# Kernel optimization log

Measured on AMD Instinct MI355X. Metric: run time of the kernel, lower is better.

Reference implementation:

```python
import jax, jax.numpy as jnp
import numpy as np

B, T, N, D, C = 32, 256, 256, 1024, 80
SIM_THRESH = 0.7
MAX_AGE = 10
W_SIM, W_IOU = 0.7, 0.3


def setup_inputs() -> dict:
    key = jax.random.key(0)
    ks = jax.random.split(key, 8)
    track_memory = jax.random.normal(ks[0], (B, T, D), jnp.float32)
    track_boxes = jax.random.uniform(ks[1], (B, T, 4), jnp.float32, 0.05, 0.95)
    track_active = jax.random.bernoulli(ks[2], 0.9, (B, T))
    track_age = jax.random.randint(ks[3], (B, T), 0, 5, jnp.int32)
    track_hits = jax.random.randint(ks[4], (B, T), 1, 10, jnp.int32)
    det_boxes = jax.random.uniform(ks[5], (B, N, 4), jnp.float32, 0.05, 0.95)
    # correlate detections with tracks so cosine similarity exceeds the
    # matching threshold for many pairs and the greedy loop does real work
    det_memory = track_memory + 0.3 * jax.random.normal(ks[6], (B, N, D), jnp.float32)
    class_logits = jax.random.normal(ks[7], (B, N, C), jnp.float32)
    return {
        'track_memory': track_memory, 'track_boxes': track_boxes,
        'track_active': track_active, 'track_age': track_age,
        'track_hits': track_hits, 'det_boxes': det_boxes,
        'det_memory': det_memory, 'class_logits': class_logits,
    }


def _normalize(x):
    # matches F.normalize(dim=-1): x / max(||x||, eps)
    n = jnp.linalg.norm(x, axis=-1, keepdims=True)
    return x / jnp.maximum(n, 1e-12)


def _iou_matrix(tb, db):
    # tb [T,4], db [N,4], boxes in (cx, cy, w, h) format -> IoU [T,N]
    t_x1, t_y1 = tb[:, 0] - tb[:, 2] / 2, tb[:, 1] - tb[:, 3] / 2
    t_x2, t_y2 = tb[:, 0] + tb[:, 2] / 2, tb[:, 1] + tb[:, 3] / 2
    d_x1, d_y1 = db[:, 0] - db[:, 2] / 2, db[:, 1] - db[:, 3] / 2
    d_x2, d_y2 = db[:, 0] + db[:, 2] / 2, db[:, 1] + db[:, 3] / 2
    iw = jnp.clip(jnp.minimum(t_x2[:, None], d_x2[None, :]) - jnp.maximum(t_x1[:, None], d_x1[None, :]), 0.0)
    ih = jnp.clip(jnp.minimum(t_y2[:, None], d_y2[None, :]) - jnp.maximum(t_y1[:, None], d_y1[None, :]), 0.0)
    inter = iw * ih
    union = (tb[:, 2] * tb[:, 3])[:, None] + (db[:, 2] * db[:, 3])[None, :] - inter
    return inter / (union + 1e-6)


def _greedy_match(Cmat):
    # sequential greedy argmax matching, as in the torch while-loop.
    # returns match_det [T]: detection index matched to each track, -1 if none.
    Tn, Nn = Cmat.shape

    def step(carry, _):
        Cm, match_det = carry
        flat = Cm.reshape(-1)
        idx = jnp.argmax(flat)
        val = flat[idx]
        ok = val >= SIM_THRESH
        t = idx // Nn
        d = idx % Nn
        match_det = jnp.where(ok, match_det.at[t].set(d.astype(jnp.int32)), match_det)
        Cm = jnp.where(ok, Cm.at[t, :].set(-1.0).at[:, d].set(-1.0), Cm)
        return (Cm, match_det), None

    init = (Cmat, jnp.full((Tn,), -1, jnp.int32))
    (_, match_det), _ = jax.lax.scan(step, init, None, length=min(Tn, Nn))
    return match_det


def reference(track_memory, track_boxes, track_active, track_age, track_hits,
              det_boxes, det_memory, class_logits):
    # detection scores (computed in torch update(); not used downstream)
    scores = jnp.max(jax.nn.softmax(class_logits, axis=-1), axis=-1)  # [B,N]

    def per_batch(tm, tb, ta, age, hits, db, dm):
        sim = _normalize(tm) @ _normalize(dm).T            # [T,N] cosine sim
        iou = _iou_matrix(tb, db)                          # [T,N]
        Cmat = W_SIM * sim + W_IOU * iou
        Cmat = jnp.where(ta[:, None], Cmat, -1.0)          # inactive rows -> -1
        match_det = _greedy_match(Cmat)                    # [T]
        matched = match_det >= 0
        d = jnp.clip(match_det, 0)
        new_mem = jnp.where(matched[:, None], dm[d], tm)
        new_box = jnp.where(matched[:, None], db[d], tb)
        new_hits = jnp.where(matched, hits + 1, hits)
        unmatched_active = ta & ~matched
        new_age = jnp.where(matched, 0, jnp.where(unmatched_active, age + 1, age))
        new_active = jnp.where(matched, True,
                               jnp.where(unmatched_active, new_age <= MAX_AGE, ta))
        return new_mem, new_box, new_active, new_age, new_hits, match_det

    new_mem, new_box, new_active, new_age, new_hits, match_det = jax.vmap(per_batch)(
        track_memory, track_boxes, track_active, track_age, track_hits,
        det_boxes, det_memory)
    return new_mem, new_box, new_active, new_age, new_hits, match_det, scores
```

## Files before the change

### kernel.cpp

```cpp
#include <hip/hip_runtime.h>
#include <math.h>

static constexpr int PB = 32, PT = 256, PN = 256, PD = 1024, PC = 80;
static constexpr int BCAP = 96;
static constexpr int CAP  = 256;
static constexpr int NT   = 16;

static constexpr size_t O_MEM   = 0;
static constexpr size_t O_BOX   = O_MEM   + (size_t)PB*PT*PD;
static constexpr size_t O_ACT   = O_BOX   + (size_t)PB*PT*4;
static constexpr size_t O_AGE   = O_ACT   + (size_t)PB*PT;
static constexpr size_t O_HITS  = O_AGE   + (size_t)PB*PT;
static constexpr size_t O_MATCH = O_HITS  + (size_t)PB*PT;
static constexpr size_t O_SCORE = O_MATCH + (size_t)PB*PT;

typedef __attribute__((ext_vector_type(8))) short short8;
typedef __attribute__((ext_vector_type(4))) float f32x4;


__device__ __forceinline__ unsigned ordbits(float f) {
    unsigned b = __float_as_uint(f);
    return (b & 0x80000000u) ? ~b : (b | 0x80000000u);
}
__device__ __forceinline__ unsigned short f2bf(float f) {
    unsigned u = __float_as_uint(f);
    unsigned r = u + 0x7fffu + ((u >> 16) & 1u);
    return (unsigned short)(r >> 16);
}
__device__ __forceinline__ short8 pack8(float4 lo, float4 hi) {
    union { unsigned u[4]; short8 s; } r;
    r.u[0] = f2bf(lo.x) | ((unsigned)f2bf(lo.y) << 16);
    r.u[1] = f2bf(lo.z) | ((unsigned)f2bf(lo.w) << 16);
    r.u[2] = f2bf(hi.x) | ((unsigned)f2bf(hi.y) << 16);
    r.u[3] = f2bf(hi.z) | ((unsigned)f2bf(hi.w) << 16);
    return r.s;
}

__device__ __forceinline__ float box_cost(float sim, float4 bt, float4 bd) {
    float tX1 = bt.x - bt.z*0.5f, tX2 = bt.x + bt.z*0.5f;
    float tY1 = bt.y - bt.w*0.5f, tY2 = bt.y + bt.w*0.5f;
    float dX1 = bd.x - bd.z*0.5f, dX2 = bd.x + bd.z*0.5f;
    float dY1 = bd.y - bd.w*0.5f, dY2 = bd.y + bd.w*0.5f;
    float iw = fmaxf(fminf(tX2, dX2) - fmaxf(tX1, dX1), 0.f);
    float ih = fmaxf(fminf(tY2, dY2) - fmaxf(tY1, dY1), 0.f);
    float inter = iw * ih;
    float iou = inter / (bt.z*bt.w + bd.z*bd.w - inter + 1e-6f);
    return 0.7f * sim + 0.3f * iou;
}

__global__ __launch_bounds__(256) void k_prep(
        const float* __restrict__ tm, const float* __restrict__ dm,
        const float* __restrict__ lg,
        short* __restrict__ abf, short* __restrict__ bbf,
        float* __restrict__ asums, float* __restrict__ bsums,
        float* __restrict__ ddots, float* __restrict__ out) {
    const int bx = blockIdx.x;
    const int tid = threadIdx.x;
    const int w = tid >> 6, lane = tid & 63;
    if (bx < PB * PT / 16) {
        const int m16 = lane & 15, quad = lane >> 4;
        const int row = bx * 16 + m16;
        const float* tp = tm + (size_t)row * PD;
        const float* dp = dm + (size_t)row * PD;
        const size_t fb = (size_t)bx * 32 * 512;
        float as = 0.f, bs = 0.f, dd = 0.f;
#pragma unroll
        for (int kq = 0; kq < 8; ++kq) {
            const int kk = w * 8 + kq;
            const int e = kk * 32 + quad * 8;
            float4 a0 = *(const float4*)(tp + e);
            float4 a1 = *(const float4*)(tp + e + 4);
            float4 d0 = *(const float4*)(dp + e);
            float4 d1 = *(const float4*)(dp + e + 4);
            as += a0.x*a0.x + a0.y*a0.y + a0.z*a0.z + a0.w*a0.w
                + a1.x*a1.x + a1.y*a1.y + a1.z*a1.z + a1.w*a1.w;
            bs += d0.x*d0.x + d0.y*d0.y + d0.z*d0.z + d0.w*d0.w
                + d1.x*d1.x + d1.y*d1.y + d1.z*d1.z + d1.w*d1.w;
            dd += a0.x*d0.x + a0.y*d0.y + a0.z*d0.z + a0.w*d0.w
                + a1.x*d1.x + a1.y*d1.y + a1.z*d1.z + a1.w*d1.w;
            *(short8*)(abf + fb + (size_t)kk * 512 + lane * 8) = pack8(a0, a1);
            *(short8*)(bbf + fb + (size_t)kk * 512 + lane * 8) = pack8(d0, d1);
        }
        as += __shfl_xor(as, 16); as += __shfl_xor(as, 32);
        bs += __shfl_xor(bs, 16); bs += __shfl_xor(bs, 32);
        dd += __shfl_xor(dd, 16); dd += __shfl_xor(dd, 32);
        __shared__ float red[3][4][16];
        if (quad == 0) { red[0][w][m16] = as; red[1][w][m16] = bs; red[2][w][m16] = dd; }
        __syncthreads();
        if (tid < 16) {
            int rg = bx * 16 + tid;
            asums[rg] = red[0][0][tid] + red[0][1][tid] + red[0][2][tid] + red[0][3][tid];
            bsums[rg] = red[1][0][tid] + red[1][1][tid] + red[1][2][tid] + red[1][3][tid];
            ddots[rg] = red[2][0][tid] + red[2][1][tid] + red[2][2][tid] + red[2][3][tid];
        }
    } else {
        int rowi = (bx - PB * PT / 16) * 4 + w;
        const float* p = lg + (size_t)rowi * PC;
        float x0 = p[lane];
        float x1 = (lane < PC - 64) ? p[64 + lane] : -INFINITY;
        float m = fmaxf(x0, x1);
#pragma unroll
        for (int o = 32; o > 0; o >>= 1) m = fmaxf(m, __shfl_down(m, o));
        m = __shfl(m, 0);
        float s = expf(x0 - m) + ((lane < PC - 64) ? expf(x1 - m) : 0.f);
#pragma unroll
        for (int o = 32; o > 0; o >>= 1) s += __shfl_down(s, o);
        if (lane == 0) out[O_SCORE + rowi] = 1.0f / s;
    }
}

__global__ __launch_bounds__(256) void k_sim(
        const short* __restrict__ abf, const short* __restrict__ bbf,
        const float* __restrict__ tb, const float* __restrict__ db,
        const unsigned* __restrict__ ta,
        const float* __restrict__ asums, const float* __restrict__ bsums,
        unsigned* __restrict__ cntblk, int* __restrict__ cand) {
    const int i = blockIdx.x;
    const int xcd = i & 7, j = i >> 3;
    const int b = xcd * 4 + (j >> 4);
    const int tile = j & 15;
    const int rowbase = (tile >> 2) * 64;
    const int colbase = (tile & 3) * 64;
    const int bid = b * NT + tile;
    const int tid = threadIdx.x;
    const int w = tid >> 6, lane = tid & 63;
    const int wm = w >> 1, wn = w & 1;
    const int m16 = lane & 15, quad = lane >> 4;

    __shared__ unsigned bcnt;
    __shared__ float ainv[64], binv[64];
    if (tid == 0) bcnt = 0u;
    if (tid < 64)
        ainv[tid] = 1.0f / fmaxf(sqrtf(asums[b * PT + rowbase + tid]), 1e-12f);
    else if (tid < 128)
        binv[tid - 64] = 1.0f / fmaxf(sqrtf(bsums[b * PN + colbase + tid - 64]), 1e-12f);

    const short8* A8 = (const short8*)abf;
    const short8* B8 = (const short8*)bbf;
    const size_t a0b = ((size_t)(b * 16 + (rowbase >> 4) + wm * 2)) * 2048 + lane;
    const size_t b0b = ((size_t)(b * 16 + (colbase >> 4) + wn * 2)) * 2048 + lane;

    f32x4 acc00 = (f32x4)0.f, acc01 = (f32x4)0.f;
    f32x4 acc10 = (f32x4)0.f, acc11 = (f32x4)0.f;
#pragma unroll 4
    for (int kk = 0; kk < 32; ++kk) {
        short8 a0 = A8[a0b + (size_t)kk * 64];
        short8 a1 = A8[a0b + (size_t)kk * 64 + 2048];
        short8 b0 = B8[b0b + (size_t)kk * 64];
        short8 b1 = B8[b0b + (size_t)kk * 64 + 2048];
        acc00 = __builtin_amdgcn_mfma_f32_16x16x32_bf16(a0, b0, acc00, 0, 0, 0);
        acc01 = __builtin_amdgcn_mfma_f32_16x16x32_bf16(a0, b1, acc01, 0, 0, 0);
        acc10 = __builtin_amdgcn_mfma_f32_16x16x32_bf16(a1, b0, acc10, 0, 0, 0);
        acc11 = __builtin_amdgcn_mfma_f32_16x16x32_bf16(a1, b1, acc11, 0, 0, 0);
    }
    f32x4 accm[2][2] = {{acc00, acc01}, {acc10, acc11}};

    __syncthreads();

    float dx1[2], dy1[2], dx2[2], dy2[2], darea[2], dnv[2];
    int ng[2];
#pragma unroll
    for (int nj = 0; nj < 2; ++nj) {
        int cl = wn * 32 + nj * 16 + m16;
        ng[nj] = colbase + cl;
        dnv[nj] = binv[cl];
        float4 bx = *(const float4*)&db[((size_t)b * PN + ng[nj]) * 4];
        dx1[nj] = bx.x - bx.z * 0.5f; dx2[nj] = bx.x + bx.z * 0.5f;
        dy1[nj] = bx.y - bx.w * 0.5f; dy2[nj] = bx.y + bx.w * 0.5f;
        darea[nj] = bx.z * bx.w;
    }

#pragma unroll
    for (int mi = 0; mi < 2; ++mi) {
#pragma unroll
        for (int r = 0; r < 4; ++r) {
            int tl = wm * 32 + mi * 16 + quad * 4 + r;
            int tg = rowbase + tl;
            if (ta[b * PT + tg] == 0u) continue;
            float tnv = ainv[tl];
            float4 bx = *(const float4*)&tb[((size_t)b * PT + tg) * 4];
            float tX1 = bx.x - bx.z * 0.5f, tX2 = bx.x + bx.z * 0.5f;
            float tY1 = bx.y - bx.w * 0.5f, tY2 = bx.y + bx.w * 0.5f;
            float tA = bx.z * bx.w;
#pragma unroll
            for (int nj = 0; nj < 2; ++nj) {
                float sim = accm[mi][nj][r] * tnv * dnv[nj];
                float iw = fmaxf(fminf(tX2, dx2[nj]) - fmaxf(tX1, dx1[nj]), 0.f);
                float ih = fmaxf(fminf(tY2, dy2[nj]) - fmaxf(tY1, dy1[nj]), 0.f);
                float inter = iw * ih;
                float iou = inter / (tA + darea[nj] - inter + 1e-6f);
                float cost = 0.7f * sim + 0.3f * iou;
                if (cost >= 0.695f) {
                    unsigned idx = atomicAdd(&bcnt, 1u);
                    if (idx < BCAP) cand[bid * BCAP + idx] = (tg << 8) | ng[nj];
                }
            }
        }
    }
    __syncthreads();
    if (tid == 0) cntblk[bid] = (bcnt > BCAP) ? BCAP : bcnt;
}

__global__ __launch_bounds__(256) void k_match(
        const float* __restrict__ tm, const float* __restrict__ dm,
        const float* __restrict__ tb, const float* __restrict__ db,
        const float* __restrict__ asums, const float* __restrict__ bsums,
        const float* __restrict__ ddots,
        const unsigned* __restrict__ cntblk, const int* __restrict__ cand,
        int* __restrict__ md) {
    const int b = blockIdx.x;
    const int tid = threadIdx.x;
    const int w = tid >> 6, lane = tid & 63;
    __shared__ int cnts[NT];
    __shared__ unsigned long long sel_key[CAP];
    __shared__ unsigned sel_cnt;
    __shared__ int odd_slot[64];
    __shared__ unsigned odd_cnt;
    __shared__ int rcnt[PT];
    __shared__ int ccnt[PN];
    __shared__ int conflict;

    if (tid == 0) { sel_cnt = 0u; odd_cnt = 0u; conflict = 0; }
    if (tid < NT) {
        int cj = (int)cntblk[b * NT + tid];
        cnts[tid] = (cj > BCAP) ? BCAP : cj;
    }
    rcnt[tid] = 0; ccnt[tid] = 0;
    md[b * PT + tid] = -1;
    __syncthreads();

    for (int u = tid; u < NT * BCAP; u += 256) {
        int j = u / BCAP, i = u - j * BCAP;
        if (i >= cnts[j]) continue;
        int gidx = (b * NT + j) * BCAP + i;
        int pair = cand[gidx];
        int t = pair >> 8, n = pair & 255;
        if (t == n) {
            float na  = asums[b * PT + t];
            float nb  = bsums[b * PN + n];
            float dot = ddots[b * PT + t];
            float sim = dot * (1.0f / fmaxf(sqrtf(na), 1e-12f))
                            * (1.0f / fmaxf(sqrtf(nb), 1e-12f));
            float4 bt = *(const float4*)&tb[((size_t)b * PT + t) * 4];
            float4 bd = *(const float4*)&db[((size_t)b * PN + n) * 4];
            float cost = box_cost(sim, bt, bd);
            if (cost >= 0.7f) {
                unsigned s = atomicAdd(&sel_cnt, 1u);
                if (s < CAP)
                    sel_key[s] = ((unsigned long long)ordbits(cost) << 16)
                               | (unsigned long long)(65535 - pair);
            }
        } else {
            unsigned oi = atomicAdd(&odd_cnt, 1u);
            if (oi < 64) odd_slot[oi] = gidx;
        }
    }
    __syncthreads();

    int nodd = (int)odd_cnt; if (nodd > 64) nodd = 64;
    for (int j = w; j < nodd; j += 4) {
        int pair = cand[odd_slot[j]];
        int t = pair >> 8, n = pair & 255;
        const float4* tr = (const float4*)(tm + ((size_t)b * PT + t) * PD);
        const float4* dr = (const float4*)(dm + ((size_t)b * PN + n) * PD);
        float dot = 0.f;
#pragma unroll
        for (int q = 0; q < 4; ++q) {
            float4 v = tr[lane + 64 * q];
            float4 u = dr[lane + 64 * q];
            dot += v.x*u.x + v.y*u.y + v.z*u.z + v.w*u.w;
        }
#pragma unroll
        for (int o = 1; o < 64; o <<= 1) dot += __shfl_xor(dot, o);
        if (lane == 0) {
            float na = asums[b * PT + t], nb = bsums[b * PN + n];
            float sim = dot * (1.0f / fmaxf(sqrtf(na), 1e-12f))
                            * (1.0f / fmaxf(sqrtf(nb), 1e-12f));
            float4 bt = *(const float4*)&tb[((size_t)b * PT + t) * 4];
            float4 bd = *(const float4*)&db[((size_t)b * PN + n) * 4];
            float cost = box_cost(sim, bt, bd);
            if (cost >= 0.7f) {
                unsigned s = atomicAdd(&sel_cnt, 1u);
                if (s < CAP)
                    sel_key[s] = ((unsigned long long)ordbits(cost) << 16)
                               | (unsigned long long)(65535 - pair);
            }
        }
    }
    __syncthreads();

    const unsigned ns = (sel_cnt > (unsigned)CAP) ? (unsigned)CAP : sel_cnt;
    for (unsigned s = tid; s < ns; s += 256) {
        int flat = 65535 - (int)(sel_key[s] & 0xFFFFull);
        if (atomicAdd(&rcnt[flat >> 8], 1) >= 1) conflict = 1;
        if (atomicAdd(&ccnt[flat & 255], 1) >= 1) conflict = 1;
    }
    __syncthreads();

    if (!conflict) {
        for (unsigned s = tid; s < ns; s += 256) {
            int flat = 65535 - (int)(sel_key[s] & 0xFFFFull);
            md[b * PT + (flat >> 8)] = flat & 255;
        }
        return;
    }

    if (w == 0) {
        unsigned long long k[4];
#pragma unroll
        for (int s = 0; s < 4; ++s) {
            unsigned idx = (unsigned)lane + 64u * s;
            k[s] = (idx < ns) ? sel_key[idx] : 0ull;
        }
        int mdv[4] = {-1, -1, -1, -1};
        for (int it = 0; it < PT; ++it) {
            unsigned long long m = k[0];
            if (k[1] > m) m = k[1];
            if (k[2] > m) m = k[2];
            if (k[3] > m) m = k[3];
#pragma unroll
            for (int o = 1; o < 64; o <<= 1) {
                unsigned long long s = __shfl_xor(m, o);
                if (s > m) m = s;
            }
            if (m == 0ull) break;
            int flat = 65535 - (int)(m & 0xFFFFull);
            int t = flat >> 8, d = flat & 255;
            if ((t & 63) == lane) mdv[t >> 6] = d;
#pragma unroll
            for (int s = 0; s < 4; ++s) {
                if (k[s]) {
                    int f2 = 65535 - (int)(k[s] & 0xFFFFull);
                    if ((f2 >> 8) == t || (f2 & 255) == d) k[s] = 0ull;
                }
            }
        }
#pragma unroll
        for (int s = 0; s < 4; ++s) md[b * PT + s * 64 + lane] = mdv[s];
    }
}

__global__ __launch_bounds__(256) void k_outsc(
        const float* __restrict__ tm, const float* __restrict__ tb,
        const unsigned* __restrict__ ta, const int* __restrict__ age,
        const int* __restrict__ hits, const float* __restrict__ db,
        const float* __restrict__ dm, const int* __restrict__ md,
        float* __restrict__ out) {
    const int w = threadIdx.x >> 6, lane = threadIdx.x & 63;
    int idx = blockIdx.x * 4 + w;
    int b = idx >> 8;
    int m = md[idx];
    bool matched = m >= 0;
    int d = matched ? m : 0;
    const float4* src = (const float4*)(matched ? dm + ((size_t)b * PN + d) * PD
                                                : tm + (size_t)idx * PD);
    float4* dst = (float4*)(out + O_MEM + (size_t)idx * PD);
#pragma unroll
    for (int q = 0; q < 4; ++q) dst[lane + 64 * q] = src[lane + 64 * q];
    if (lane < 4) {
        const float* sb = matched ? db + ((size_t)b * PN + d) * 4
                                  : tb + (size_t)idx * 4;
        out[O_BOX + (size_t)idx * 4 + lane] = sb[lane];
    }
    if (lane == 0) {
        bool tact = ta[idx] != 0u;
        int hh = hits[idx], ag = age[idx];
        int nh = matched ? hh + 1 : hh;
        bool unm = tact && !matched;
        int na = matched ? 0 : (unm ? ag + 1 : ag);
        bool nact = matched ? true : (unm ? (na <= 10) : tact);
        out[O_ACT   + idx] = nact ? 1.0f : 0.0f;
        out[O_AGE   + idx] = (float)na;
        out[O_HITS  + idx] = (float)nh;
        out[O_MATCH + idx] = (float)m;
    }
}

extern "C" void kernel_launch(void* const* d_in, const int* in_sizes, int n_in,
                              void* d_out, int out_size, void* d_ws, size_t ws_size,
                              hipStream_t stream) {
    const float*    tm   = (const float*)d_in[0];
    const float*    tb   = (const float*)d_in[1];
    const unsigned* ta   = (const unsigned*)d_in[2];
    const int*      age  = (const int*)d_in[3];
    const int*      hits = (const int*)d_in[4];
    const float*    db   = (const float*)d_in[5];
    const float*    dm   = (const float*)d_in[6];
    const float*    lg   = (const float*)d_in[7];
    float* out = (float*)d_out;

    char* ws = (char*)d_ws;
    short* abf   = (short*)ws;
    short* bbf   = abf + (size_t)PB * PT * PD;
    float* asums = (float*)(bbf + (size_t)PB * PN * PD);
    float* bsums = asums + PB * PT;
    float* ddots = bsums + PB * PN;
    unsigned* cntblk = (unsigned*)(ddots + PB * PT);
    int* cand = (int*)(cntblk + PB * NT);
    int* md   = cand + PB * NT * BCAP;

    k_prep <<<PB * PT / 16 + PB * PN / 4, 256, 0, stream>>>(
        tm, dm, lg, abf, bbf, asums, bsums, ddots, out);
    k_sim  <<<PB * NT, 256, 0, stream>>>(
        abf, bbf, tb, db, ta, asums, bsums, cntblk, cand);
    k_match<<<dim3(PB), 256, 0, stream>>>(
        tm, dm, tb, db, asums, bsums, ddots, cntblk, cand, md);
    k_outsc<<<PB * PT / 4, 256, 0, stream>>>(
        tm, tb, ta, age, hits, db, dm, md, out);
}
```

Measured before the change: 155.9 us.

## Double block size to 512 threads across prep, sim and match kernels

Raises the block size of k_prep, k_sim and k_match from 256 to 512 threads. k_prep now splits the K dimension over 8 waves, and k_sim gives each wave a 16x32 output tile with register double-buffered fragment loads. The goal is more waves per block for latency hiding, plus shorter per-wave serial loops in the memory-bound prep and in the GEMM. In exchange, each k_sim wave reuses its loaded A and B fragments across fewer MFMAs, and k_match carries more threads than its serial tail can use.

```diff
diff --git a/kernel.cpp b/kernel.cpp
--- a/kernel.cpp
+++ b/kernel.cpp
@@ -48,7 +48,7 @@
     return 0.7f * sim + 0.3f * iou;
 }
 
-__global__ __launch_bounds__(256) void k_prep(
+__global__ __launch_bounds__(512) void k_prep(
         const float* __restrict__ tm, const float* __restrict__ dm,
         const float* __restrict__ lg,
         short* __restrict__ abf, short* __restrict__ bbf,
@@ -65,8 +65,8 @@
         const size_t fb = (size_t)bx * 32 * 512;
         float as = 0.f, bs = 0.f, dd = 0.f;
 #pragma unroll
-        for (int kq = 0; kq < 8; ++kq) {
-            const int kk = w * 8 + kq;
+        for (int kq = 0; kq < 4; ++kq) {
+            const int kk = w * 4 + kq;
             const int e = kk * 32 + quad * 8;
             float4 a0 = *(const float4*)(tp + e);
             float4 a1 = *(const float4*)(tp + e + 4);
@@ -84,17 +84,20 @@
         as += __shfl_xor(as, 16); as += __shfl_xor(as, 32);
         bs += __shfl_xor(bs, 16); bs += __shfl_xor(bs, 32);
         dd += __shfl_xor(dd, 16); dd += __shfl_xor(dd, 32);
-        __shared__ float red[3][4][16];
+        __shared__ float red[3][8][16];
         if (quad == 0) { red[0][w][m16] = as; red[1][w][m16] = bs; red[2][w][m16] = dd; }
         __syncthreads();
         if (tid < 16) {
             int rg = bx * 16 + tid;
-            asums[rg] = red[0][0][tid] + red[0][1][tid] + red[0][2][tid] + red[0][3][tid];
-            bsums[rg] = red[1][0][tid] + red[1][1][tid] + red[1][2][tid] + red[1][3][tid];
-            ddots[rg] = red[2][0][tid] + red[2][1][tid] + red[2][2][tid] + red[2][3][tid];
+            float s0 = 0.f, s1 = 0.f, s2 = 0.f;
+#pragma unroll
+            for (int j = 0; j < 8; ++j) {
+                s0 += red[0][j][tid]; s1 += red[1][j][tid]; s2 += red[2][j][tid];
+            }
+            asums[rg] = s0; bsums[rg] = s1; ddots[rg] = s2;
         }
     } else {
-        int rowi = (bx - PB * PT / 16) * 4 + w;
+        int rowi = (bx - PB * PT / 16) * 8 + w;
         const float* p = lg + (size_t)rowi * PC;
         float x0 = p[lane];
         float x1 = (lane < PC - 64) ? p[64 + lane] : -INFINITY;
@@ -109,7 +112,7 @@
     }
 }
 
-__global__ __launch_bounds__(256) void k_sim(
+__global__ __launch_bounds__(512) void k_sim(
         const short* __restrict__ abf, const short* __restrict__ bbf,
         const float* __restrict__ tb, const float* __restrict__ db,
         const unsigned* __restrict__ ta,
@@ -124,7 +127,7 @@
     const int bid = b * NT + tile;
     const int tid = threadIdx.x;
     const int w = tid >> 6, lane = tid & 63;
-    const int wm = w >> 1, wn = w & 1;
+    const int wm = w & 3, wn = w >> 2;
     const int m16 = lane & 15, quad = lane >> 4;
 
     __shared__ unsigned bcnt;
@@ -137,23 +140,25 @@
 
     const short8* A8 = (const short8*)abf;
     const short8* B8 = (const short8*)bbf;
-    const size_t a0b = ((size_t)(b * 16 + (rowbase >> 4) + wm * 2)) * 2048 + lane;
-    const size_t b0b = ((size_t)(b * 16 + (colbase >> 4) + wn * 2)) * 2048 + lane;
-
-    f32x4 acc00 = (f32x4)0.f, acc01 = (f32x4)0.f;
-    f32x4 acc10 = (f32x4)0.f, acc11 = (f32x4)0.f;
-#pragma unroll 4
-    for (int kk = 0; kk < 32; ++kk) {
-        short8 a0 = A8[a0b + (size_t)kk * 64];
-        short8 a1 = A8[a0b + (size_t)kk * 64 + 2048];
-        short8 b0 = B8[b0b + (size_t)kk * 64];
-        short8 b1 = B8[b0b + (size_t)kk * 64 + 2048];
-        acc00 = __builtin_amdgcn_mfma_f32_16x16x32_bf16(a0, b0, acc00, 0, 0, 0);
-        acc01 = __builtin_amdgcn_mfma_f32_16x16x32_bf16(a0, b1, acc01, 0, 0, 0);
-        acc10 = __builtin_amdgcn_mfma_f32_16x16x32_bf16(a1, b0, acc10, 0, 0, 0);
-        acc11 = __builtin_amdgcn_mfma_f32_16x16x32_bf16(a1, b1, acc11, 0, 0, 0);
-    }
-    f32x4 accm[2][2] = {{acc00, acc01}, {acc10, acc11}};
+    const size_t ab = ((size_t)(b * 16 + (rowbase >> 4) + wm)) * 2048 + lane;
+    const size_t bbse = ((size_t)(b * 16 + (colbase >> 4) + wn * 2)) * 2048 + lane;
+
+    f32x4 acc0 = (f32x4)0.f, acc1 = (f32x4)0.f;
+    short8 av  = A8[ab];
+    short8 b0v = B8[bbse];
+    short8 b1v = B8[bbse + 2048];
+#pragma unroll
+    for (int kk = 0; kk < 31; ++kk) {
+        const size_t o = (size_t)(kk + 1) * 64;
+        short8 na  = A8[ab + o];
+        short8 nb0 = B8[bbse + o];
+        short8 nb1 = B8[bbse + o + 2048];
+        acc0 = __builtin_amdgcn_mfma_f32_16x16x32_bf16(av, b0v, acc0, 0, 0, 0);
+        acc1 = __builtin_amdgcn_mfma_f32_16x16x32_bf16(av, b1v, acc1, 0, 0, 0);
+        av = na; b0v = nb0; b1v = nb1;
+    }
+    acc0 = __builtin_amdgcn_mfma_f32_16x16x32_bf16(av, b0v, acc0, 0, 0, 0);
+    acc1 = __builtin_amdgcn_mfma_f32_16x16x32_bf16(av, b1v, acc1, 0, 0, 0);
 
     __syncthreads();
 
@@ -171,29 +176,26 @@
     }
 
 #pragma unroll
-    for (int mi = 0; mi < 2; ++mi) {
-#pragma unroll
-        for (int r = 0; r < 4; ++r) {
-            int tl = wm * 32 + mi * 16 + quad * 4 + r;
-            int tg = rowbase + tl;
-            if (ta[b * PT + tg] == 0u) continue;
-            float tnv = ainv[tl];
-            float4 bx = *(const float4*)&tb[((size_t)b * PT + tg) * 4];
-            float tX1 = bx.x - bx.z * 0.5f, tX2 = bx.x + bx.z * 0.5f;
-            float tY1 = bx.y - bx.w * 0.5f, tY2 = bx.y + bx.w * 0.5f;
-            float tA = bx.z * bx.w;
-#pragma unroll
-            for (int nj = 0; nj < 2; ++nj) {
-                float sim = accm[mi][nj][r] * tnv * dnv[nj];
-                float iw = fmaxf(fminf(tX2, dx2[nj]) - fmaxf(tX1, dx1[nj]), 0.f);
-                float ih = fmaxf(fminf(tY2, dy2[nj]) - fmaxf(tY1, dy1[nj]), 0.f);
-                float inter = iw * ih;
-                float iou = inter / (tA + darea[nj] - inter + 1e-6f);
-                float cost = 0.7f * sim + 0.3f * iou;
-                if (cost >= 0.695f) {
-                    unsigned idx = atomicAdd(&bcnt, 1u);
-                    if (idx < BCAP) cand[bid * BCAP + idx] = (tg << 8) | ng[nj];
-                }
+    for (int r = 0; r < 4; ++r) {
+        int tl = wm * 16 + quad * 4 + r;
+        int tg = rowbase + tl;
+        if (ta[b * PT + tg] == 0u) continue;
+        float tnv = ainv[tl];
+        float4 bx = *(const float4*)&tb[((size_t)b * PT + tg) * 4];
+        float tX1 = bx.x - bx.z * 0.5f, tX2 = bx.x + bx.z * 0.5f;
+        float tY1 = bx.y - bx.w * 0.5f, tY2 = bx.y + bx.w * 0.5f;
+        float tA = bx.z * bx.w;
+#pragma unroll
+        for (int nj = 0; nj < 2; ++nj) {
+            float sim = (nj == 0 ? acc0[r] : acc1[r]) * tnv * dnv[nj];
+            float iw = fmaxf(fminf(tX2, dx2[nj]) - fmaxf(tX1, dx1[nj]), 0.f);
+            float ih = fmaxf(fminf(tY2, dy2[nj]) - fmaxf(tY1, dy1[nj]), 0.f);
+            float inter = iw * ih;
+            float iou = inter / (tA + darea[nj] - inter + 1e-6f);
+            float cost = 0.7f * sim + 0.3f * iou;
+            if (cost >= 0.695f) {
+                unsigned idx = atomicAdd(&bcnt, 1u);
+                if (idx < BCAP) cand[bid * BCAP + idx] = (tg << 8) | ng[nj];
             }
         }
     }
@@ -201,7 +203,7 @@
     if (tid == 0) cntblk[bid] = (bcnt > BCAP) ? BCAP : bcnt;
 }
 
-__global__ __launch_bounds__(256) void k_match(
+__global__ __launch_bounds__(512) void k_match(
         const float* __restrict__ tm, const float* __restrict__ dm,
         const float* __restrict__ tb, const float* __restrict__ db,
         const float* __restrict__ asums, const float* __restrict__ bsums,
@@ -225,11 +227,11 @@
         int cj = (int)cntblk[b * NT + tid];
         cnts[tid] = (cj > BCAP) ? BCAP : cj;
     }
-    rcnt[tid] = 0; ccnt[tid] = 0;
-    md[b * PT + tid] = -1;
-    __syncthreads();
-
-    for (int u = tid; u < NT * BCAP; u += 256) {
+    if (tid < PT) { rcnt[tid] = 0; md[b * PT + tid] = -1; }
+    if (tid < PN) ccnt[tid] = 0;
+    __syncthreads();
+
+    for (int u = tid; u < NT * BCAP; u += 512) {
         int j = u / BCAP, i = u - j * BCAP;
         if (i >= cnts[j]) continue;
         int gidx = (b * NT + j) * BCAP + i;
@@ -258,7 +260,7 @@
     __syncthreads();
 
     int nodd = (int)odd_cnt; if (nodd > 64) nodd = 64;
-    for (int j = w; j < nodd; j += 4) {
+    for (int j = w; j < nodd; j += 8) {
         int pair = cand[odd_slot[j]];
         int t = pair >> 8, n = pair & 255;
         const float4* tr = (const float4*)(tm + ((size_t)b * PT + t) * PD);
@@ -290,7 +292,7 @@
     __syncthreads();
 
     const unsigned ns = (sel_cnt > (unsigned)CAP) ? (unsigned)CAP : sel_cnt;
-    for (unsigned s = tid; s < ns; s += 256) {
+    for (unsigned s = tid; s < ns; s += 512) {
         int flat = 65535 - (int)(sel_key[s] & 0xFFFFull);
         if (atomicAdd(&rcnt[flat >> 8], 1) >= 1) conflict = 1;
         if (atomicAdd(&ccnt[flat & 255], 1) >= 1) conflict = 1;
@@ -298,7 +300,7 @@
     __syncthreads();
 
     if (!conflict) {
-        for (unsigned s = tid; s < ns; s += 256) {
+        for (unsigned s = tid; s < ns; s += 512) {
             int flat = 65535 - (int)(sel_key[s] & 0xFFFFull);
             md[b * PT + (flat >> 8)] = flat & 255;
         }
@@ -399,11 +401,11 @@
     int* cand = (int*)(cntblk + PB * NT);
     int* md   = cand + PB * NT * BCAP;
 
-    k_prep <<<PB * PT / 16 + PB * PN / 4, 256, 0, stream>>>(
+    k_prep <<<PB * PT / 16 + PB * PN / 8, 512, 0, stream>>>(
         tm, dm, lg, abf, bbf, asums, bsums, ddots, out);
-    k_sim  <<<PB * NT, 256, 0, stream>>>(
+    k_sim  <<<PB * NT, 512, 0, stream>>>(
         abf, bbf, tb, db, ta, asums, bsums, cntblk, cand);
-    k_match<<<dim3(PB), 256, 0, stream>>>(
+    k_match<<<dim3(PB), 512, 0, stream>>>(
         tm, dm, tb, db, asums, bsums, ddots, cntblk, cand, md);
     k_outsc<<<PB * PT / 4, 256, 0, stream>>>(
         tm, tb, ta, age, hits, db, dm, md, out);
```

After: 154.8 us (median of 2 runs). Within noise of the previous version (-0.7%).
